# Performance work log

Hardware: AMD Instinct MI355X
Metric: run time of the kernel (lower is better)

## Reference

```python
import jax, jax.numpy as jnp
import numpy as np

D_IN = 1024
D_OUT = 1024
B, S = 4, 2048

def setup_inputs() -> dict:
    key = jax.random.key(0)
    ks = jax.random.split(key, 7)
    s_in = 1.0 / np.sqrt(D_IN)
    return {
        "X": jax.random.normal(ks[0], (B, S, D_IN), dtype=jnp.float32),
        "Wq": jax.random.uniform(ks[1], (D_OUT, D_IN), jnp.float32, -s_in, s_in),
        "bq": jax.random.uniform(ks[2], (D_OUT,), jnp.float32, -s_in, s_in),
        "Wk": jax.random.uniform(ks[3], (D_OUT, D_IN), jnp.float32, -s_in, s_in),
        "bk": jax.random.uniform(ks[4], (D_OUT,), jnp.float32, -s_in, s_in),
        "Wv": jax.random.uniform(ks[5], (D_OUT, D_IN), jnp.float32, -s_in, s_in),
        "bv": jax.random.uniform(ks[6], (D_OUT,), jnp.float32, -s_in, s_in),
    }

def reference(X, Wq, bq, Wk, bk, Wv, bv):
    # Linear projections (torch Linear: x @ W.T + b)
    q = X @ Wq.T + bq            # [B, S, D_OUT]
    k = X @ Wk.T + bk
    v = X @ Wv.T + bv
    scores = jnp.einsum("bqd,bkd->bqk", q, k) / jnp.sqrt(jnp.float32(D_OUT))
    seq = scores.shape[-1]
    causal = jnp.tril(jnp.ones((seq, seq), dtype=bool))  # True where allowed
    scores = jnp.where(causal, scores, -jnp.inf)
    attn = jax.nn.softmax(scores, axis=-1)
    return jnp.einsum("bqk,bkd->bqd", attn, v)
```

## Files before the change

kernel.cpp:

```cpp
#include <hip/hip_runtime.h>
#include <hip/hip_bf16.h>


typedef __attribute__((ext_vector_type(8))) short short8;
typedef __attribute__((ext_vector_type(4))) float floatx4;

#define SEQ   2048
#define DMODEL 1024
#define NBATCH 4
#define MTOT  (SEQ * NBATCH)

__device__ __forceinline__ void stage16(const __hip_bfloat16* g, __hip_bfloat16* l)
{
  __builtin_amdgcn_global_load_lds(
      (const __attribute__((address_space(1))) void*)g,
      (__attribute__((address_space(3))) void*)l, 16, 0, 0);
}

__device__ __forceinline__ unsigned short bf16_bits(float f)
{
  __hip_bfloat16 h = __float2bfloat16(f);
  return *(unsigned short*)&h;
}

__global__ __launch_bounds__(256) void convert_all(
    const float* __restrict__ X,  const float* __restrict__ Wq,
    const float* __restrict__ Wk, const float* __restrict__ Wv,
    __hip_bfloat16* __restrict__ Xb,  __hip_bfloat16* __restrict__ Wqb,
    __hip_bfloat16* __restrict__ Wkb, __hip_bfloat16* __restrict__ Wvb)
{
  const int b = blockIdx.x;
  const float* src; __hip_bfloat16* dst; int rel;
  if (b < 8192)       { src = X;  dst = Xb;  rel = b; }
  else if (b < 9216)  { src = Wq; dst = Wqb; rel = b - 8192; }
  else if (b < 10240) { src = Wk; dst = Wkb; rel = b - 9216; }
  else                { src = Wv; dst = Wvb; rel = b - 10240; }
  const int i = rel * 1024 + threadIdx.x * 4;
  float4 f = *(const float4*)(src + i);
  uint2 o;
  o.x = (unsigned)bf16_bits(f.x) | ((unsigned)bf16_bits(f.y) << 16);
  o.y = (unsigned)bf16_bits(f.z) | ((unsigned)bf16_bits(f.w) << 16);
  *(uint2*)(dst + i) = o;
}

__global__ __launch_bounds__(256, 2) void gemm_qkv_fused(
    const __hip_bfloat16* __restrict__ Xb,
    const __hip_bfloat16* __restrict__ Wqb,
    const __hip_bfloat16* __restrict__ Wkb,
    const __hip_bfloat16* __restrict__ Wvb,
    const float* __restrict__ bq, const float* __restrict__ bk, const float* __restrict__ bv,
    __hip_bfloat16* __restrict__ Qb, __hip_bfloat16* __restrict__ Kb, __hip_bfloat16* __restrict__ Vt)
{
  __shared__ __hip_bfloat16 As[128 * 32];
  __shared__ __hip_bfloat16 Bs[3][128 * 32];
  const int m0 = blockIdx.y * 128, n0 = blockIdx.x * 128;
  const int tid  = threadIdx.x;
  const int lane = tid & 63;
  const int wave = tid >> 6;
  const int quad = lane >> 4;
  const int r    = lane & 15;
  const int wm   = (wave >> 1) * 64;
  const int wn   = (wave & 1) * 64;
  const int srow = wave * 16 + (lane >> 2);
  const int scol = (lane & 3) * 8;

  const __hip_bfloat16* Wp[3] = {Wqb, Wkb, Wvb};

  __hip_bfloat16* lA0 = As + wave * 512;
  __hip_bfloat16* lA1 = As + 2048 + wave * 512;

  const __hip_bfloat16* aR0 = Xb + (size_t)(m0 + srow) * DMODEL + scol;
  const __hip_bfloat16* aR1 = aR0 + (size_t)64 * DMODEL;

  floatx4 acc[3][4][4] = {};

  for (int kt = 0; kt < DMODEL / 32; ++kt) {
    const int k0 = kt * 32;
    stage16(aR0 + k0, lA0);
    stage16(aR1 + k0, lA1);
#pragma unroll
    for (int w = 0; w < 3; ++w) {
      stage16(Wp[w] + (size_t)(n0 + srow) * DMODEL + scol + k0,      Bs[w] + wave * 512);
      stage16(Wp[w] + (size_t)(n0 + 64 + srow) * DMODEL + scol + k0, Bs[w] + 2048 + wave * 512);
    }
    __syncthreads();
    short8 a[4];
#pragma unroll
    for (int i = 0; i < 4; ++i)
      a[i] = *(const short8*)(As + (wm + i * 16 + r) * 32 + quad * 8);
#pragma unroll
    for (int w = 0; w < 3; ++w) {
      short8 b[4];
#pragma unroll
      for (int j = 0; j < 4; ++j)
        b[j] = *(const short8*)(Bs[w] + (wn + j * 16 + r) * 32 + quad * 8);
#pragma unroll
      for (int i = 0; i < 4; ++i)
#pragma unroll
        for (int j = 0; j < 4; ++j)
          acc[w][i][j] = __builtin_amdgcn_mfma_f32_16x16x32_bf16(a[i], b[j], acc[w][i][j], 0, 0, 0);
    }
    __syncthreads();
  }

  {
    __hip_bfloat16* Op[2] = {Qb, Kb};
    const float* Bp[2] = {bq, bk};
#pragma unroll
    for (int w = 0; w < 2; ++w) {
      __hip_bfloat16* out = Op[w];
#pragma unroll
      for (int j = 0; j < 4; ++j) {
        const int n = n0 + wn + j * 16 + r;
        const float bb = Bp[w][n];
#pragma unroll
        for (int i = 0; i < 4; ++i) {
          const int mbase = m0 + wm + i * 16 + quad * 4;
#pragma unroll
          for (int e = 0; e < 4; ++e)
            out[(size_t)(mbase + e) * DMODEL + n] = __float2bfloat16(acc[w][i][j][e] + bb);
        }
      }
    }
  }
  {
    const int z    = m0 >> 11;
    const int posb = (m0 & (SEQ - 1)) + wm;
    __hip_bfloat16* vt = Vt + (size_t)z * DMODEL * SEQ;
#pragma unroll
    for (int j = 0; j < 4; ++j) {
      const int n = n0 + wn + j * 16 + r;
      const float bb = bv[n];
#pragma unroll
      for (int i = 0; i < 4; ++i) {
        const int pos = posb + i * 16 + quad * 4;
        unsigned long long pk =
            (unsigned long long)bf16_bits(acc[2][i][j][0] + bb)
          | ((unsigned long long)bf16_bits(acc[2][i][j][1] + bb) << 16)
          | ((unsigned long long)bf16_bits(acc[2][i][j][2] + bb) << 32)
          | ((unsigned long long)bf16_bits(acc[2][i][j][3] + bb) << 48);
        *(unsigned long long*)(vt + (size_t)n * SEQ + pos) = pk;
      }
    }
  }
}

template <bool SUMS>
__device__ __forceinline__ void gemm_core_2w(
    const __hip_bfloat16* __restrict__ A,
    const __hip_bfloat16* __restrict__ B,
    int K, int m0, int n0, int kchunks,
    __hip_bfloat16* As , __hip_bfloat16* Bs ,
    floatx4 acc[4][4], floatx4 acc_s[4])
{
  const int tid  = threadIdx.x;
  const int lane = tid & 63;
  const int wave = tid >> 6;
  const int quad = lane >> 4;
  const int r    = lane & 15;
  const int wn   = wave * 64;
  const int lrow = lane >> 2;
  const int lcol = (lane & 3) * 8;

  short8 ones;
#pragma unroll
  for (int t = 0; t < 8; ++t) ones[t] = (short)0x3F80;

  const __hip_bfloat16* aB = A + (size_t)(m0 + wave * 32 + lrow) * K + lcol;
  const __hip_bfloat16* bB = B + (size_t)(n0 + wave * 64 + lrow) * K + lcol;
  __hip_bfloat16* lA = As + wave * 1024;
  __hip_bfloat16* lB = Bs + wave * 2048;

  for (int kt = 0; kt < kchunks; ++kt) {
    const int k0 = kt * 32;
#pragma unroll
    for (int s = 0; s < 2; ++s)
      stage16(aB + (size_t)(16 * s) * K + k0, lA + s * 512);
#pragma unroll
    for (int s = 0; s < 4; ++s)
      stage16(bB + (size_t)(16 * s) * K + k0, lB + s * 512);
    __syncthreads();
    short8 a[4], b[4];
#pragma unroll
    for (int i = 0; i < 4; ++i) {
      a[i] = *(const short8*)(As + (i * 16 + r) * 32 + quad * 8);
      b[i] = *(const short8*)(Bs + (wn + i * 16 + r) * 32 + quad * 8);
    }
    if (SUMS) {
#pragma unroll
      for (int i = 0; i < 4; ++i)
        acc_s[i] = __builtin_amdgcn_mfma_f32_16x16x32_bf16(a[i], ones, acc_s[i], 0, 0, 0);
    }
#pragma unroll
    for (int i = 0; i < 4; ++i)
#pragma unroll
      for (int j = 0; j < 4; ++j)
        acc[i][j] = __builtin_amdgcn_mfma_f32_16x16x32_bf16(a[i], b[j], acc[i][j], 0, 0, 0);
    __syncthreads();
  }
}

__global__ __launch_bounds__(128, 4) void gemm_scores(
    const __hip_bfloat16* __restrict__ Qb, const __hip_bfloat16* __restrict__ Kb,
    __hip_bfloat16* __restrict__ Sb)
{
  const int z = blockIdx.y;
  const int L = blockIdx.x;
  int p = (int)((sqrtf(4.0f * (float)L + 1.0f) - 1.0f) * 0.5f);
  while ((p + 1) * (p + 2) <= L) ++p;
  while (p * (p + 1) > L) --p;
  const int o  = L - p * (p + 1);
  const int mt = 2 * p + (o > p ? 1 : 0);
  const int nt = (o > p) ? (o - p - 1) : o;
  const int m0 = mt * 64, n0 = nt * 128;

  __shared__ __hip_bfloat16 As[64 * 32], Bs[128 * 32];
  const __hip_bfloat16* A = Qb + (size_t)z * SEQ * DMODEL;
  const __hip_bfloat16* B = Kb + (size_t)z * SEQ * DMODEL;
  __hip_bfloat16* outp = Sb + (size_t)z * SEQ * SEQ;
  floatx4 acc[4][4] = {};
  floatx4 dummy[4];
  gemm_core_2w<false>(A, B, DMODEL, m0, n0, DMODEL / 32, As, Bs, acc, dummy);

  const int lane = threadIdx.x & 63, wave = threadIdx.x >> 6;
  const int quad = lane >> 4, r = lane & 15;
  const int wn = wave * 64;
  const float scale = 0.03125f;
#pragma unroll
  for (int i = 0; i < 4; ++i) {
    const int mbase = m0 + i * 16 + quad * 4;
#pragma unroll
    for (int e = 0; e < 4; ++e) {
      const int row = mbase + e;
#pragma unroll
      for (int j = 0; j < 4; ++j) {
        const int n = n0 + wn + j * 16 + r;
        const float pv = (n <= row) ? __expf(acc[i][j][e] * scale) : 0.f;
        outp[(size_t)row * SEQ + n] = __float2bfloat16(pv);
      }
    }
  }
}

__global__ __launch_bounds__(128, 4) void gemm_pv(
    const __hip_bfloat16* __restrict__ Sb, const __hip_bfloat16* __restrict__ Vt,
    float* __restrict__ Out)
{
  __shared__ __hip_bfloat16 As[64 * 32], Bs[128 * 32];
  const int z = blockIdx.z;
  const int mt = (int)gridDim.y - 1 - (int)blockIdx.y;
  const int m0 = mt * 64, n0 = blockIdx.x * 128;
  const __hip_bfloat16* A = Sb + (size_t)z * SEQ * SEQ;
  const __hip_bfloat16* B = Vt + (size_t)z * DMODEL * SEQ;
  float* outp = Out + (size_t)z * SEQ * DMODEL;

  floatx4 acc[4][4] = {};
  floatx4 acc_s[4] = {};
  const int kchunks = 2 * mt + 2;
  gemm_core_2w<true>(A, B, SEQ, m0, n0, kchunks, As, Bs, acc, acc_s);

  const int lane = threadIdx.x & 63, wave = threadIdx.x >> 6;
  const int quad = lane >> 4, r = lane & 15;
  const int wn = wave * 64;
#pragma unroll
  for (int i = 0; i < 4; ++i) {
    const int mbase = m0 + i * 16 + quad * 4;
    float inv[4];
#pragma unroll
    for (int e = 0; e < 4; ++e) inv[e] = 1.f / acc_s[i][e];
#pragma unroll
    for (int j = 0; j < 4; ++j) {
      const int n = n0 + wn + j * 16 + r;
#pragma unroll
      for (int e = 0; e < 4; ++e)
        outp[(size_t)(mbase + e) * DMODEL + n] = acc[i][j][e] * inv[e];
    }
  }
}

extern "C" void kernel_launch(void* const* d_in, const int* in_sizes, int n_in,
                              void* d_out, int out_size, void* d_ws, size_t ws_size,
                              hipStream_t stream)
{
  const float* X  = (const float*)d_in[0];
  const float* Wq = (const float*)d_in[1];
  const float* bq = (const float*)d_in[2];
  const float* Wk = (const float*)d_in[3];
  const float* bk = (const float*)d_in[4];
  const float* Wv = (const float*)d_in[5];
  const float* bv = (const float*)d_in[6];
  float* Out = (float*)d_out;

  char* ws = (char*)d_ws;
  size_t off = 0;
  auto alloc = [&](size_t bytes) -> void* {
    void* p = ws + off;
    off += (bytes + 255) & ~(size_t)255;
    return p;
  };
  __hip_bfloat16* Xb  = (__hip_bfloat16*)alloc((size_t)MTOT * DMODEL * 2);
  __hip_bfloat16* Wqb = (__hip_bfloat16*)alloc((size_t)DMODEL * DMODEL * 2);
  __hip_bfloat16* Wkb = (__hip_bfloat16*)alloc((size_t)DMODEL * DMODEL * 2);
  __hip_bfloat16* Wvb = (__hip_bfloat16*)alloc((size_t)DMODEL * DMODEL * 2);
  __hip_bfloat16* Qb  = (__hip_bfloat16*)alloc((size_t)MTOT * DMODEL * 2);
  __hip_bfloat16* Kb  = (__hip_bfloat16*)alloc((size_t)MTOT * DMODEL * 2);
  __hip_bfloat16* Vt  = (__hip_bfloat16*)alloc((size_t)MTOT * DMODEL * 2);
  __hip_bfloat16* Sb  = (__hip_bfloat16*)alloc((size_t)NBATCH * SEQ * SEQ * 2);
  (void)ws_size; (void)in_sizes; (void)n_in; (void)out_size;

  convert_all<<<11264, 256, 0, stream>>>(X, Wq, Wk, Wv, Xb, Wqb, Wkb, Wvb);
  gemm_qkv_fused<<<dim3(DMODEL / 128, MTOT / 128), 256, 0, stream>>>(
      Xb, Wqb, Wkb, Wvb, bq, bk, bv, Qb, Kb, Vt);
  gemm_scores<<<dim3(272, NBATCH), 128, 0, stream>>>(Qb, Kb, Sb);
  gemm_pv<<<dim3(DMODEL / 128, SEQ / 64, NBATCH), 128, 0, stream>>>(Sb, Vt, Out);
}
```

Measured before the change: 247.7 us.

## Store Q and K as FP8 and compute attention scores with FP8 MFMA

Q and K projections are written as FP8 e4m3 bytes instead of bf16. The scores GEMM now uses a new FP8 core that stages 64-wide K chunks into LDS and issues fp8 MFMA instructions. This halves Q/K storage and load traffic and uses the higher-throughput FP8 matrix path. The cost is reduced precision in the scores, which are then exponentiated without max subtraction, so accuracy tolerance may be at risk.

```diff
diff --git a/kernel.cpp b/kernel.cpp
--- a/kernel.cpp
+++ b/kernel.cpp
@@ -1,16 +1,18 @@
 #include <hip/hip_runtime.h>
 #include <hip/hip_bf16.h>
+#include <hip/hip_fp8.h>
 
 
 typedef __attribute__((ext_vector_type(8))) short short8;
 typedef __attribute__((ext_vector_type(4))) float floatx4;
+typedef __attribute__((ext_vector_type(2))) long longx2;
 
 #define SEQ   2048
 #define DMODEL 1024
 #define NBATCH 4
 #define MTOT  (SEQ * NBATCH)
 
-__device__ __forceinline__ void stage16(const __hip_bfloat16* g, __hip_bfloat16* l)
+__device__ __forceinline__ void stage16(const void* g, void* l)
 {
   __builtin_amdgcn_global_load_lds(
       (const __attribute__((address_space(1))) void*)g,
@@ -21,6 +23,12 @@
 {
   __hip_bfloat16 h = __float2bfloat16(f);
   return *(unsigned short*)&h;
+}
+
+__device__ __forceinline__ unsigned char fp8_bits(float f)
+{
+  __hip_fp8_e4m3 h(f);
+  return h.__x;
 }
 
 __global__ __launch_bounds__(256) void convert_all(
@@ -49,7 +57,8 @@
     const __hip_bfloat16* __restrict__ Wkb,
     const __hip_bfloat16* __restrict__ Wvb,
     const float* __restrict__ bq, const float* __restrict__ bk, const float* __restrict__ bv,
-    __hip_bfloat16* __restrict__ Qb, __hip_bfloat16* __restrict__ Kb, __hip_bfloat16* __restrict__ Vt)
+    unsigned char* __restrict__ Qb, unsigned char* __restrict__ Kb,
+    __hip_bfloat16* __restrict__ Vt)
 {
   __shared__ __hip_bfloat16 As[128 * 32];
   __shared__ __hip_bfloat16 Bs[3][128 * 32];
@@ -104,11 +113,11 @@
   }
 
   {
-    __hip_bfloat16* Op[2] = {Qb, Kb};
+    unsigned char* Op[2] = {Qb, Kb};
     const float* Bp[2] = {bq, bk};
 #pragma unroll
     for (int w = 0; w < 2; ++w) {
-      __hip_bfloat16* out = Op[w];
+      unsigned char* out = Op[w];
 #pragma unroll
       for (int j = 0; j < 4; ++j) {
         const int n = n0 + wn + j * 16 + r;
@@ -118,7 +127,7 @@
           const int mbase = m0 + wm + i * 16 + quad * 4;
 #pragma unroll
           for (int e = 0; e < 4; ++e)
-            out[(size_t)(mbase + e) * DMODEL + n] = __float2bfloat16(acc[w][i][j][e] + bb);
+            out[(size_t)(mbase + e) * DMODEL + n] = fp8_bits(acc[w][i][j][e] + bb);
         }
       }
     }
@@ -145,6 +154,54 @@
   }
 }
 
+__device__ __forceinline__ void gemm_core_2w_fp8(
+    const unsigned char* __restrict__ A,
+    const unsigned char* __restrict__ B,
+    int K, int m0, int n0, int kchunks,
+    unsigned char* As , unsigned char* Bs ,
+    floatx4 acc[4][4])
+{
+  const int tid  = threadIdx.x;
+  const int lane = tid & 63;
+  const int wave = tid >> 6;
+  const int quad = lane >> 4;
+  const int r    = lane & 15;
+  const int wn   = wave * 64;
+  const int lrow = lane >> 2;
+  const int lcol = (lane & 3) * 16;
+
+  const unsigned char* aB = A + (size_t)(m0 + wave * 32 + lrow) * K + lcol;
+  const unsigned char* bB = B + (size_t)(n0 + wave * 64 + lrow) * K + lcol;
+  unsigned char* lA = As + wave * 2048;
+  unsigned char* lB = Bs + wave * 4096;
+
+  for (int kt = 0; kt < kchunks; ++kt) {
+    const int k0 = kt * 64;
+#pragma unroll
+    for (int s = 0; s < 2; ++s)
+      stage16(aB + (size_t)(16 * s) * K + k0, lA + s * 1024);
+#pragma unroll
+    for (int s = 0; s < 4; ++s)
+      stage16(bB + (size_t)(16 * s) * K + k0, lB + s * 1024);
+    __syncthreads();
+    longx2 a[4], b[4];
+#pragma unroll
+    for (int i = 0; i < 4; ++i) {
+      a[i] = __builtin_bit_cast(longx2, *(const int4*)(As + (i * 16 + r) * 64 + quad * 16));
+      b[i] = __builtin_bit_cast(longx2, *(const int4*)(Bs + (wn + i * 16 + r) * 64 + quad * 16));
+    }
+#pragma unroll
+    for (int kk = 0; kk < 2; ++kk)
+#pragma unroll
+      for (int i = 0; i < 4; ++i)
+#pragma unroll
+        for (int j = 0; j < 4; ++j)
+          acc[i][j] = __builtin_amdgcn_mfma_f32_16x16x32_fp8_fp8(
+              a[i][kk], b[j][kk], acc[i][j], 0, 0, 0);
+    __syncthreads();
+  }
+}
+
 template <bool SUMS>
 __device__ __forceinline__ void gemm_core_2w(
     const __hip_bfloat16* __restrict__ A,
@@ -201,7 +258,7 @@
 }
 
 __global__ __launch_bounds__(128, 4) void gemm_scores(
-    const __hip_bfloat16* __restrict__ Qb, const __hip_bfloat16* __restrict__ Kb,
+    const unsigned char* __restrict__ Qb, const unsigned char* __restrict__ Kb,
     __hip_bfloat16* __restrict__ Sb)
 {
   const int z = blockIdx.y;
@@ -214,13 +271,12 @@
   const int nt = (o > p) ? (o - p - 1) : o;
   const int m0 = mt * 64, n0 = nt * 128;
 
-  __shared__ __hip_bfloat16 As[64 * 32], Bs[128 * 32];
-  const __hip_bfloat16* A = Qb + (size_t)z * SEQ * DMODEL;
-  const __hip_bfloat16* B = Kb + (size_t)z * SEQ * DMODEL;
+  __shared__ unsigned char As[64 * 64], Bs[128 * 64];
+  const unsigned char* A = Qb + (size_t)z * SEQ * DMODEL;
+  const unsigned char* B = Kb + (size_t)z * SEQ * DMODEL;
   __hip_bfloat16* outp = Sb + (size_t)z * SEQ * SEQ;
   floatx4 acc[4][4] = {};
-  floatx4 dummy[4];
-  gemm_core_2w<false>(A, B, DMODEL, m0, n0, DMODEL / 32, As, Bs, acc, dummy);
+  gemm_core_2w_fp8(A, B, DMODEL, m0, n0, DMODEL / 64, As, Bs, acc);
 
   const int lane = threadIdx.x & 63, wave = threadIdx.x >> 6;
   const int quad = lane >> 4, r = lane & 15;
@@ -302,8 +358,8 @@
   __hip_bfloat16* Wqb = (__hip_bfloat16*)alloc((size_t)DMODEL * DMODEL * 2);
   __hip_bfloat16* Wkb = (__hip_bfloat16*)alloc((size_t)DMODEL * DMODEL * 2);
   __hip_bfloat16* Wvb = (__hip_bfloat16*)alloc((size_t)DMODEL * DMODEL * 2);
-  __hip_bfloat16* Qb  = (__hip_bfloat16*)alloc((size_t)MTOT * DMODEL * 2);
-  __hip_bfloat16* Kb  = (__hip_bfloat16*)alloc((size_t)MTOT * DMODEL * 2);
+  unsigned char*  Qb  = (unsigned char*)alloc((size_t)MTOT * DMODEL);
+  unsigned char*  Kb  = (unsigned char*)alloc((size_t)MTOT * DMODEL);
   __hip_bfloat16* Vt  = (__hip_bfloat16*)alloc((size_t)MTOT * DMODEL * 2);
   __hip_bfloat16* Sb  = (__hip_bfloat16*)alloc((size_t)NBATCH * SEQ * SEQ * 2);
   (void)ws_size; (void)in_sizes; (void)n_in; (void)out_size;
```

Measured after the change: 233.5 us. -5.7%, faster.
